# Kernel tuning notes

Hardware: AMD Instinct MI355X
Metric: run time of the kernel (lower is better)

## Reference

```python
import jax, jax.numpy as jnp
import numpy as np

NUM_HEADS = 16
NEG_INF = -1e30  # finite large negative; avoids NaN on fully-masked padded query rows


def setup_inputs() -> dict:
    key = jax.random.key(0)
    k0, k1, k2, k3 = jax.random.split(key, 4)
    B, S, E = 4, 2048, 1024
    x_padded = jax.random.normal(k0, (B, S, E), dtype=jnp.float32)
    # variable lengths in [S//2, S] so no batch row is fully empty
    seq_lengths = jax.random.randint(k1, (B,), S // 2, S + 1).astype(jnp.int32)
    Wqkv = jax.random.normal(k2, (3 * E, E), dtype=jnp.float32) * 0.02  # torch Linear weight [out,in]
    Wout = jax.random.normal(k3, (E, E), dtype=jnp.float32) * 0.02
    return {"x_padded": x_padded, "Wqkv": Wqkv, "Wout": Wout,
            "seq_lengths": seq_lengths, "window_left": 512, "window_right": 0}


def _build_mask(seq_lengths, S, window_left, window_right):
    # key-side padding mask: [B, S]
    pad = jnp.arange(S)[None, :] < seq_lengths[:, None]
    mask = pad[:, None, None, :]  # [B,1,1,S]
    if window_left >= 0 or window_right >= 0:
        i = jnp.arange(S)[:, None]
        j = jnp.arange(S)[None, :]
        win = jnp.ones((S, S), dtype=bool)
        if window_left >= 0:
            win = win & (j >= i - window_left)
        if window_right >= 0:
            win = win & (j <= i + window_right)
        mask = mask & win[None, None, :, :]
    elif (window_left, window_right) == (-1, 0):
        causal = jnp.tril(jnp.ones((S, S), dtype=bool))
        mask = mask & causal[None, None, :, :]
    return mask  # [B,1,S,S] (broadcasts over heads)


def reference(x_padded, Wqkv, Wout, seq_lengths, window_left, window_right):
    B, S, E = x_padded.shape
    H = NUM_HEADS
    D = E // H
    scale = 1.0 / jnp.sqrt(jnp.float32(D))
    qkv = x_padded @ Wqkv.T  # [B,S,3E]
    q, k, v = jnp.split(qkv, 3, axis=-1)
    q = q.reshape(B, S, H, D).transpose(0, 2, 1, 3)  # [B,H,S,D]
    k = k.reshape(B, S, H, D).transpose(0, 2, 1, 3)
    v = v.reshape(B, S, H, D).transpose(0, 2, 1, 3)
    mask = _build_mask(seq_lengths, S, window_left, window_right)
    scores = jnp.einsum("bhid,bhjd->bhij", q, k) * scale
    scores = jnp.where(mask, scores, NEG_INF)
    attn = jax.nn.softmax(scores, axis=-1)
    out = jnp.einsum("bhij,bhjd->bhid", attn, v)  # [B,H,S,D]
    out = out.transpose(0, 2, 1, 3).reshape(B, S, E)
    return out @ Wout.T
```

## Files before the change

### kernel.cpp

```cpp
#include <hip/hip_runtime.h>

typedef __bf16 bf16;
typedef __attribute__((ext_vector_type(2))) __bf16 bf16x2;
typedef __attribute__((ext_vector_type(4))) __bf16 bf16x4;
typedef __attribute__((ext_vector_type(8))) __bf16 bf16x8;
typedef __attribute__((ext_vector_type(4))) float f32x4;
typedef __attribute__((ext_vector_type(16))) float f32x16;

#define B_ 4
#define S_ 2048
#define H_ 16
#define D_ 64
#define E_ 1024

#define BM 256
#define BN 128
#define BK 64

__device__ __forceinline__ int imin(int a, int b) { return a < b ? a : b; }
__device__ __forceinline__ int imax(int a, int b) { return a > b ? a : b; }

__device__ __forceinline__ void gload_lds16(const void* g, void* l) {
  __builtin_amdgcn_global_load_lds(
      (const __attribute__((address_space(1))) void*)g,
      (__attribute__((address_space(3))) void*)l, 16, 0, 0);
}

__global__ __launch_bounds__(256) void cvt3_kernel(
    const float* __restrict__ x, bf16* __restrict__ xb,
    const float* __restrict__ wqkv, bf16* __restrict__ wqkvb,
    const float* __restrict__ wout, bf16* __restrict__ woutb) {
  const int bid = blockIdx.x;
  const float* in;
  bf16* out;
  int idx;
  if (bid < 4096) { in = x; out = xb; idx = bid; }
  else if (bid < 5632) { in = wqkv; out = wqkvb; idx = bid - 4096; }
  else { in = wout; out = woutb; idx = bid - 5632; }
  const int i = (idx * 256 + threadIdx.x) * 8;
  float4 v0 = *(const float4*)(in + i);
  float4 v1 = *(const float4*)(in + i + 4);
  bf16x8 o;
  o[0] = (bf16)v0.x; o[1] = (bf16)v0.y; o[2] = (bf16)v0.z; o[3] = (bf16)v0.w;
  o[4] = (bf16)v1.x; o[5] = (bf16)v1.y; o[6] = (bf16)v1.z; o[7] = (bf16)v1.w;
  *(bf16x8*)(out + i) = o;
}

__global__ __launch_bounds__(512, 1) void gemm_pipe(
    const bf16* __restrict__ A, const bf16* __restrict__ Bm,
    int M, int N, int K, int mode,
    bf16* __restrict__ qd, bf16* __restrict__ kd, bf16* __restrict__ vtd,
    float* __restrict__ outf) {
  __shared__ __align__(16) bf16 As[3][BM * BK];
  __shared__ __align__(16) bf16 Bs[3][BN * BK];
  const int tid = threadIdx.x;
  const int wave = tid >> 6, lane = tid & 63;
  const int l15 = lane & 15, l4 = lane >> 4;
  const int wm = (wave >> 1) * 64;
  const int wn = (wave & 1) * 64;

  const int nwg = gridDim.x * gridDim.y;
  const int fid = blockIdx.y * gridDim.x + blockIdx.x;
  const int chunk = nwg >> 3;
  const int swz = (fid & 7) * chunk + (fid >> 3);
  const int tn = swz % gridDim.x;
  const int tm = swz / gridDim.x;

  const bf16* Abase = A + (size_t)tm * BM * K;
  const bf16* Bbase = Bm + (size_t)tn * BN * K;

  f32x4 acc[4][4];
#pragma unroll
  for (int i = 0; i < 4; ++i)
#pragma unroll
    for (int j = 0; j < 4; ++j)
#pragma unroll
      for (int r = 0; r < 4; ++r) acc[i][j][r] = 0.f;

  const int NT = K >> 6;

#define STAGE_A(sbuf, k0)                                                      \
  {                                                                            \
    _Pragma("unroll") for (int ld = 0; ld < 4; ++ld) {                         \
      const int idx = ld * 512 + tid;                                          \
      const int row = idx >> 3, g = idx & 7;                                   \
      const int gs = g ^ (row & 7);                                            \
      gload_lds16(Abase + (size_t)row * K + (k0) + gs * 8,                     \
                  As[sbuf] + (ld * 512 + wave * 64) * 8);                      \
    }                                                                          \
  }
#define STAGE_B(sbuf, k0)                                                      \
  {                                                                            \
    _Pragma("unroll") for (int ld = 0; ld < 2; ++ld) {                         \
      const int idx = ld * 512 + tid;                                          \
      const int row = idx >> 3, g = idx & 7;                                   \
      const int gs = g ^ (row & 7);                                            \
      gload_lds16(Bbase + (size_t)row * K + (k0) + gs * 8,                     \
                  Bs[sbuf] + (ld * 512 + wave * 64) * 8);                      \
    }                                                                          \
  }

  STAGE_A(0, 0); STAGE_B(0, 0);
  STAGE_A(1, BK); STAGE_B(1, BK);
  asm volatile("s_waitcnt vmcnt(6)" ::: "memory");
  __builtin_amdgcn_s_barrier();

  int p = 0;
  for (int t = 0; t < NT; ++t) {
    const bf16* Ap = As[p];
    const bf16* Bp = Bs[p];
    const int sb = (p + 2 >= 3) ? p - 1 : p + 2;
    const int sk0 = ((t + 2 < NT) ? t + 2 : NT - 1) * BK;

    bf16x8 a[4], bfr[4];
#pragma unroll
    for (int i = 0; i < 4; ++i) {
      const int ra = wm + i * 16 + l15;
      a[i] = *(const bf16x8*)(Ap + ra * 64 + ((l4 ^ (ra & 7)) * 8));
      const int rb = wn + i * 16 + l15;
      bfr[i] = *(const bf16x8*)(Bp + rb * 64 + ((l4 ^ (rb & 7)) * 8));
    }
    STAGE_A(sb, sk0);
    __builtin_amdgcn_s_setprio(1);
#pragma unroll
    for (int i = 0; i < 4; ++i)
#pragma unroll
      for (int j = 0; j < 4; ++j)
        acc[i][j] = __builtin_amdgcn_mfma_f32_16x16x32_bf16(a[i], bfr[j],
                                                            acc[i][j], 0, 0, 0);
    __builtin_amdgcn_s_setprio(0);
#pragma unroll
    for (int i = 0; i < 4; ++i) {
      const int ra = wm + i * 16 + l15;
      a[i] = *(const bf16x8*)(Ap + ra * 64 + (((4 + l4) ^ (ra & 7)) * 8));
      const int rb = wn + i * 16 + l15;
      bfr[i] = *(const bf16x8*)(Bp + rb * 64 + (((4 + l4) ^ (rb & 7)) * 8));
    }
    STAGE_B(sb, sk0);
    __builtin_amdgcn_s_setprio(1);
#pragma unroll
    for (int i = 0; i < 4; ++i)
#pragma unroll
      for (int j = 0; j < 4; ++j)
        acc[i][j] = __builtin_amdgcn_mfma_f32_16x16x32_bf16(a[i], bfr[j],
                                                            acc[i][j], 0, 0, 0);
    __builtin_amdgcn_s_setprio(0);

    asm volatile("s_waitcnt vmcnt(6)" ::: "memory");
    __builtin_amdgcn_s_barrier();
    p = (p + 1 >= 3) ? 0 : p + 1;
  }
#undef STAGE_A
#undef STAGE_B

  if (mode == 0) {
#pragma unroll
    for (int i = 0; i < 4; ++i) {
      const int m0 = tm * BM + wm + i * 16 + l4 * 4;
      const int b = m0 >> 11, s = m0 & (S_ - 1);
#pragma unroll
      for (int j = 0; j < 4; ++j) {
        const int n = tn * BN + wn + j * 16 + l15;
        const int which = n >> 10;
        const int hn = n & 1023;
        const int h = hn >> 6, d = hn & 63;
        const f32x4 av = acc[i][j];
        if (which == 0) {
#pragma unroll
          for (int r = 0; r < 4; ++r)
            qd[((size_t)(b * H_ + h) * S_ + (s + r)) * D_ + d] =
                (bf16)(av[r] * 0.125f);
        } else if (which == 1) {
#pragma unroll
          for (int r = 0; r < 4; ++r)
            kd[((size_t)(b * H_ + h) * S_ + (s + r)) * D_ + d] = (bf16)av[r];
        } else {
          bf16x4 pv;
#pragma unroll
          for (int r = 0; r < 4; ++r) pv[r] = (bf16)av[r];
          *(bf16x4*)(vtd + ((size_t)(b * H_ + h) * D_ + d) * S_ + s) = pv;
        }
      }
    }
  } else {
#pragma unroll
    for (int i = 0; i < 4; ++i) {
      const int m0 = tm * BM + wm + i * 16 + l4 * 4;
#pragma unroll
      for (int j = 0; j < 4; ++j) {
        const int n = tn * BN + wn + j * 16 + l15;
#pragma unroll
        for (int r = 0; r < 4; ++r) outf[(size_t)(m0 + r) * N + n] = acc[i][j][r];
      }
    }
  }
}

__global__ __launch_bounds__(256) void meanv_kernel(const bf16* __restrict__ vt,
                                                    float* __restrict__ meanv) {
  const int bh = blockIdx.x >> 2, dq = blockIdx.x & 3;
  const int tid = threadIdx.x;
  const int dl = tid >> 4;
  const int sl = tid & 15;
  const int d = dq * 16 + dl;
  const bf16* row = vt + ((size_t)bh * D_ + d) * S_;
  float s = 0.f;
#pragma unroll
  for (int it = 0; it < 16; ++it) {
    bf16x8 v = *(const bf16x8*)(row + it * 128 + sl * 8);
#pragma unroll
    for (int j = 0; j < 8; ++j) s += (float)v[j];
  }
#pragma unroll
  for (int m = 1; m < 16; m <<= 1) s += __shfl_xor(s, m, 64);
  if (sl == 0) meanv[(size_t)bh * D_ + d] = s * (1.0f / (float)S_);
}

__device__ __forceinline__ int pk2(float a, float b) {
  union { bf16x2 h; int i; } u;
  u.h[0] = (bf16)a; u.h[1] = (bf16)b;
  return u.i;
}

__global__ __launch_bounds__(256) void attn_kernel(
    const bf16* __restrict__ q, const bf16* __restrict__ k,
    const bf16* __restrict__ vt, const float* __restrict__ meanv,
    const int* __restrict__ seq_lengths, const int* __restrict__ wlp,
    const int* __restrict__ wrp, bf16* __restrict__ attn_out) {
  __shared__ __align__(16) bf16 Ks[2][128 * 64];
  __shared__ __align__(16) bf16 Vs[2][64 * 128];
  const int tid = threadIdx.x, wave = tid >> 6, lane = tid & 63;
  const int l31 = lane & 31, l5 = lane >> 5;
  const int bid0 = blockIdx.x;
  const int bid = (bid0 & 7) * 64 + (bid0 >> 3);
  const int bh = bid >> 3;
  const int gp = bid & 7;
  const int b = bh >> 4, h = bh & 15;
  const int seq_len = seq_lengths[b];
  const int wl = wlp[0], wr = wrp[0];

  const bf16* qbase = q + (size_t)bh * S_ * D_;
  const bf16* kbase = k + (size_t)bh * S_ * D_;
  const bf16* vtb = vt + (size_t)bh * D_ * S_;

#define STAGE(bufb, kt0)                                                       \
  {                                                                            \
    _Pragma("unroll") for (int ld = 0; ld < 4; ++ld) {                         \
      const int idx = ld * 256 + tid;                                          \
      const int krow_i = idx >> 3, kg_ = idx & 7;                              \
      const int kgs = kg_ ^ (krow_i & 7);                                      \
      const int krow = imin((kt0) + krow_i, S_ - 1);                           \
      gload_lds16(kbase + (size_t)krow * 64 + kgs * 8, Ks[bufb] + idx * 8);    \
      const int vrow = idx >> 4, vg_ = idx & 15;                               \
      const int vgs = vg_ ^ (vrow & 15);                                       \
      const int vcol = imin((kt0) + vgs * 8, S_ - 8);                          \
      gload_lds16(vtb + (size_t)vrow * S_ + vcol, Vs[bufb] + idx * 8);         \
    }                                                                          \
  }
#define LDS_K(bufb, row, gran)                                                 \
  (*(const bf16x8*)((const char*)(Ks[bufb]) + (row) * 128 +                    \
                    (((gran) ^ ((row) & 7)) << 4)))
#define LDS_V(bufb, row, gran)                                                 \
  (*(const bf16x8*)((const char*)(Vs[bufb]) + (row) * 256 +                    \
                    (((gran) ^ ((row) & 15)) << 4)))

  for (int seg = 0; seg < 2; ++seg) {
    const int g = seg ? (15 - gp) : gp;
    const int q0b = g * 128;
    const int q0w = q0b + wave * 32;

    bf16x8 qa[4];
#pragma unroll
    for (int dg = 0; dg < 4; ++dg)
      qa[dg] = *(const bf16x8*)(qbase + (size_t)(q0w + l31) * D_ +
                                dg * 16 + l5 * 8);

    const int hi_blk = (wr >= 0) ? imin(q0b + 127 + wr, S_ - 1) : (S_ - 1);
    const int end_blk = imin(hi_blk + 1, seq_len);
    const int lo_blk = (wl >= 0) ? imax(0, q0b - wl) : 0;
    const int beg_blk = lo_blk & ~127;
    const int ntb = (end_blk > beg_blk) ? ((end_blk - beg_blk + 127) >> 7) : 0;

    const int w_hi = (wr >= 0) ? (q0w + 31 + wr) : (S_ - 1);
    const int w_end = imin(w_hi + 1, seq_len);
    const int w_lo = (wl >= 0) ? imax(0, q0w - wl) : 0;

    f32x16 o0, o1;
#pragma unroll
    for (int r = 0; r < 16; ++r) { o0[r] = 0.f; o1[r] = 0.f; }
    float mrun = -1e30f, lrun = 0.f;

    if (ntb > 0) STAGE(0, beg_blk);
    __syncthreads();

    for (int t = 0; t < ntb; ++t) {
      const int kt = beg_blk + t * 128;
      if (t + 1 < ntb) STAGE((t + 1) & 1, kt + 128);
      const int bufb = t & 1;

#pragma unroll
      for (int kk = 0; kk < 2; ++kk) {
        const int kts = kt + kk * 64;
        const bool active = (kts < w_end) && (kts + 63 >= w_lo);
        if (active) {
          f32x16 sf0, sf1;
#pragma unroll
          for (int r = 0; r < 16; ++r) { sf0[r] = 0.f; sf1[r] = 0.f; }
#pragma unroll
          for (int dg = 0; dg < 4; ++dg) {
            bf16x8 kb0 = LDS_K(bufb, kk * 64 + l31, dg * 2 + l5);
            bf16x8 kb1 = LDS_K(bufb, kk * 64 + 32 + l31, dg * 2 + l5);
            sf0 = __builtin_amdgcn_mfma_f32_32x32x16_bf16(kb0, qa[dg], sf0,
                                                          0, 0, 0);
            sf1 = __builtin_amdgcn_mfma_f32_32x32x16_bf16(kb1, qa[dg], sf1,
                                                          0, 0, 0);
          }

          bool allv = (kts + 63 < seq_len);
          if (wr >= 0) allv = allv && (kts + 63 <= q0w + wr);
          if (wl >= 0) allv = allv && (kts >= q0w + 31 - wl);
          if (!allv) {
            const int qrow = q0w + l31;
#pragma unroll
            for (int hh = 0; hh < 2; ++hh)
#pragma unroll
              for (int r = 0; r < 16; ++r) {
                const int key = kts + hh * 32 + (r & 3) + 8 * (r >> 2) + 4 * l5;
                bool valid = (key < seq_len);
                if (wr >= 0) valid = valid && (key <= qrow + wr);
                if (wl >= 0) valid = valid && (key >= qrow - wl);
                if (hh == 0) sf0[r] = valid ? sf0[r] : -1e30f;
                else sf1[r] = valid ? sf1[r] : -1e30f;
              }
          }
          float tmax = -1e30f;
#pragma unroll
          for (int r = 0; r < 16; ++r) {
            tmax = fmaxf(tmax, sf0[r]);
            tmax = fmaxf(tmax, sf1[r]);
          }
          tmax = fmaxf(tmax, __shfl_xor(tmax, 32, 64));

          if (!__all(tmax <= mrun + 8.0f)) {
            const float mnew = fmaxf(mrun, tmax);
            const float corr = __expf(mrun - mnew);
            mrun = mnew;
            lrun *= corr;
#pragma unroll
            for (int r = 0; r < 16; ++r) { o0[r] *= corr; o1[r] *= corr; }
          }

          float lsum = 0.f;
#pragma unroll
          for (int r = 0; r < 16; ++r) {
            const float e0 = (sf0[r] <= -1e29f) ? 0.f : __expf(sf0[r] - mrun);
            const float e1 = (sf1[r] <= -1e29f) ? 0.f : __expf(sf1[r] - mrun);
            sf0[r] = e0; sf1[r] = e1;
            lsum += e0 + e1;
          }
          lsum += __shfl_xor(lsum, 32, 64);
          lrun += lsum;

          bf16x8 pb[4];
#pragma unroll
          for (int kg = 0; kg < 4; ++kg) {
            const int base = (kg & 1) * 8;
            float p0, p1, p2, p3, p4, p5, p6, p7;
            if (kg < 2) {
              p0 = sf0[base + 0]; p1 = sf0[base + 1]; p2 = sf0[base + 2];
              p3 = sf0[base + 3]; p4 = sf0[base + 4]; p5 = sf0[base + 5];
              p6 = sf0[base + 6]; p7 = sf0[base + 7];
            } else {
              p0 = sf1[base + 0]; p1 = sf1[base + 1]; p2 = sf1[base + 2];
              p3 = sf1[base + 3]; p4 = sf1[base + 4]; p5 = sf1[base + 5];
              p6 = sf1[base + 6]; p7 = sf1[base + 7];
            }
            const int w0 = pk2(p0, p1);
            const int w1 = pk2(p2, p3);
            const int w2 = pk2(p4, p5);
            const int w3 = pk2(p6, p7);
            auto r02 = __builtin_amdgcn_permlane32_swap(w0, w2, false, false);
            auto r13 = __builtin_amdgcn_permlane32_swap(w1, w3, false, false);
            union { int i[4]; bf16x8 v; } u;
            u.i[0] = r02[0]; u.i[1] = r13[0]; u.i[2] = r02[1]; u.i[3] = r13[1];
            pb[kg] = u.v;
          }

#pragma unroll
          for (int kg = 0; kg < 4; ++kg) {
            bf16x8 va0 = LDS_V(bufb, l31, kk * 8 + kg * 2 + l5);
            bf16x8 va1 = LDS_V(bufb, 32 + l31, kk * 8 + kg * 2 + l5);
            o0 = __builtin_amdgcn_mfma_f32_32x32x16_bf16(va0, pb[kg], o0,
                                                         0, 0, 0);
            o1 = __builtin_amdgcn_mfma_f32_32x32x16_bf16(va1, pb[kg], o1,
                                                         0, 0, 0);
          }
        }
      }
      __syncthreads();
    }

    const int qrow = q0w + l31;
    bf16* outp = attn_out + ((size_t)(b * S_ + qrow)) * E_ + h * 64;
    if (lrun > 0.f) {
      const float inv = 1.0f / lrun;
#pragma unroll
      for (int dg2 = 0; dg2 < 2; ++dg2) {
        const f32x16& o = dg2 ? o1 : o0;
#pragma unroll
        for (int rg = 0; rg < 4; ++rg) {
          const int d0 = dg2 * 32 + 8 * rg + 4 * l5;
          bf16x4 ov;
#pragma unroll
          for (int j = 0; j < 4; ++j) ov[j] = (bf16)(o[rg * 4 + j] * inv);
          *(bf16x4*)(outp + d0) = ov;
        }
      }
    } else {
      const float* mv = meanv + (size_t)bh * D_;
#pragma unroll
      for (int dg2 = 0; dg2 < 2; ++dg2)
#pragma unroll
        for (int rg = 0; rg < 4; ++rg) {
          const int d0 = dg2 * 32 + 8 * rg + 4 * l5;
          bf16x4 ov;
#pragma unroll
          for (int j = 0; j < 4; ++j) ov[j] = (bf16)mv[d0 + j];
          *(bf16x4*)(outp + d0) = ov;
        }
    }
    __syncthreads();
  }
#undef STAGE
#undef LDS_K
#undef LDS_V
}

extern "C" void kernel_launch(void* const* d_in, const int* in_sizes, int n_in,
                              void* d_out, int out_size, void* d_ws, size_t ws_size,
                              hipStream_t stream) {
  const float* x = (const float*)d_in[0];
  const float* Wqkv = (const float*)d_in[1];
  const float* Wout = (const float*)d_in[2];
  const int* seq_lengths = (const int*)d_in[3];
  const int* wl = (const int*)d_in[4];
  const int* wr = (const int*)d_in[5];
  float* out = (float*)d_out;

  char* ws = (char*)d_ws;
  bf16* xb = (bf16*)ws;      ws += (size_t)8192 * 1024 * 2;
  bf16* wqkvb = (bf16*)ws;   ws += (size_t)3072 * 1024 * 2;
  bf16* woutb = (bf16*)ws;   ws += (size_t)1024 * 1024 * 2;
  bf16* qd = (bf16*)ws;      ws += (size_t)B_ * H_ * S_ * D_ * 2;
  bf16* kd = (bf16*)ws;      ws += (size_t)B_ * H_ * S_ * D_ * 2;
  bf16* vtd = (bf16*)ws;     ws += (size_t)B_ * H_ * S_ * D_ * 2;
  bf16* attn = (bf16*)ws;    ws += (size_t)8192 * 1024 * 2;
  float* meanv = (float*)ws; ws += (size_t)B_ * H_ * D_ * 4;

  cvt3_kernel<<<6144, 256, 0, stream>>>(x, xb, Wqkv, wqkvb, Wout, woutb);

  gemm_pipe<<<dim3(24, 32), 512, 0, stream>>>(xb, wqkvb, 8192, 3072, 1024, 0,
                                              qd, kd, vtd, nullptr);
  meanv_kernel<<<256, 256, 0, stream>>>(vtd, meanv);
  attn_kernel<<<512, 256, 0, stream>>>(qd, kd, vtd, meanv, seq_lengths, wl, wr,
                                       attn);
  gemm_pipe<<<dim3(8, 32), 512, 0, stream>>>(attn, woutb, 8192, 1024, 1024, 1,
                                             nullptr, nullptr, nullptr, out);
}
```

Before: 159.5 us.

## Fuse fp32-to-bf16 conversion of x into the QKV GEMM A-tile load

Stops converting the activation x to bf16 in a separate pass. The new QKV GEMM loads fp32 A tiles into registers, converts them and writes swizzled bf16 to LDS, while B still uses direct global-to-LDS loads. It also uses a custom tile-to-block mapping. This saves a 32MB fp32 read plus a 16MB bf16 write/read round trip, at the cost of double the A bytes per tile inside the GEMM, extra register pressure and VALU conversion work in the main loop.

Measured after the change: 179.6 us. +12.6%, slower.

```diff
diff --git a/kernel.cpp b/kernel.cpp
--- a/kernel.cpp
+++ b/kernel.cpp
@@ -26,17 +26,15 @@
       (__attribute__((address_space(3))) void*)l, 16, 0, 0);
 }
 
-__global__ __launch_bounds__(256) void cvt3_kernel(
-    const float* __restrict__ x, bf16* __restrict__ xb,
+__global__ __launch_bounds__(256) void cvt2_kernel(
     const float* __restrict__ wqkv, bf16* __restrict__ wqkvb,
     const float* __restrict__ wout, bf16* __restrict__ woutb) {
   const int bid = blockIdx.x;
   const float* in;
   bf16* out;
   int idx;
-  if (bid < 4096) { in = x; out = xb; idx = bid; }
-  else if (bid < 5632) { in = wqkv; out = wqkvb; idx = bid - 4096; }
-  else { in = wout; out = woutb; idx = bid - 5632; }
+  if (bid < 1536) { in = wqkv; out = wqkvb; idx = bid; }
+  else { in = wout; out = woutb; idx = bid - 1536; }
   const int i = (idx * 256 + threadIdx.x) * 8;
   float4 v0 = *(const float4*)(in + i);
   float4 v1 = *(const float4*)(in + i + 4);
@@ -44,6 +42,166 @@
   o[0] = (bf16)v0.x; o[1] = (bf16)v0.y; o[2] = (bf16)v0.z; o[3] = (bf16)v0.w;
   o[4] = (bf16)v1.x; o[5] = (bf16)v1.y; o[6] = (bf16)v1.z; o[7] = (bf16)v1.w;
   *(bf16x8*)(out + i) = o;
+}
+
+__global__ __launch_bounds__(512, 1) void gemm_qkv(
+    const float* __restrict__ A, const bf16* __restrict__ Bm,
+    int K,
+    bf16* __restrict__ qd, bf16* __restrict__ kd, bf16* __restrict__ vtd) {
+  __shared__ __align__(16) bf16 As[3][BM * BK];
+  __shared__ __align__(16) bf16 Bs[3][BN * BK];
+  const int tid = threadIdx.x;
+  const int wave = tid >> 6, lane = tid & 63;
+  const int l15 = lane & 15, l4 = lane >> 4;
+  const int wm = (wave >> 1) * 64;
+  const int wn = (wave & 1) * 64;
+
+  const int fid = blockIdx.y * gridDim.x + blockIdx.x;
+  const int x = fid & 7;
+  const int j = fid >> 3;
+  const int tm = (x & 3) * 8 + (j / 12);
+  const int tn = (x >> 2) * 12 + (j % 12);
+
+  const float* Abase = A + (size_t)tm * BM * K;
+  const bf16* Bbase = Bm + (size_t)tn * BN * K;
+
+  f32x4 acc[4][4];
+#pragma unroll
+  for (int i = 0; i < 4; ++i)
+#pragma unroll
+    for (int jj = 0; jj < 4; ++jj)
+#pragma unroll
+      for (int r = 0; r < 4; ++r) acc[i][jj][r] = 0.f;
+
+  const int NT = K >> 6;
+
+  float4 areg[4][2];
+
+#define LOADA(k0)                                                              \
+  {                                                                            \
+    _Pragma("unroll") for (int ld = 0; ld < 4; ++ld) {                         \
+      const int idx = ld * 512 + tid;                                          \
+      const int row = idx >> 3, g = idx & 7;                                   \
+      const int gs = g ^ (row & 7);                                            \
+      const float* src = Abase + (size_t)row * K + (k0) + gs * 8;              \
+      areg[ld][0] = *(const float4*)(src);                                     \
+      areg[ld][1] = *(const float4*)(src + 4);                                 \
+    }                                                                          \
+  }
+#define WRITEA(sbuf)                                                           \
+  {                                                                            \
+    _Pragma("unroll") for (int ld = 0; ld < 4; ++ld) {                         \
+      const int idx = ld * 512 + tid;                                          \
+      bf16x8 o;                                                                \
+      o[0] = (bf16)areg[ld][0].x; o[1] = (bf16)areg[ld][0].y;                  \
+      o[2] = (bf16)areg[ld][0].z; o[3] = (bf16)areg[ld][0].w;                  \
+      o[4] = (bf16)areg[ld][1].x; o[5] = (bf16)areg[ld][1].y;                  \
+      o[6] = (bf16)areg[ld][1].z; o[7] = (bf16)areg[ld][1].w;                  \
+      *(bf16x8*)(As[sbuf] + (size_t)idx * 8) = o;                              \
+    }                                                                          \
+  }
+#define STAGE_B(sbuf, k0)                                                      \
+  {                                                                            \
+    _Pragma("unroll") for (int ld = 0; ld < 2; ++ld) {                         \
+      const int idx = ld * 512 + tid;                                          \
+      const int row = idx >> 3, g = idx & 7;                                   \
+      const int gs = g ^ (row & 7);                                            \
+      gload_lds16(Bbase + (size_t)row * K + (k0) + gs * 8,                     \
+                  Bs[sbuf] + (ld * 512 + wave * 64) * 8);                      \
+    }                                                                          \
+  }
+
+  LOADA(0);
+  asm volatile("s_waitcnt vmcnt(0)" ::: "memory");
+  WRITEA(0);
+  LOADA(BK);
+  STAGE_B(0, 0);
+  STAGE_B(1, BK);
+  asm volatile("s_waitcnt vmcnt(4)" ::: "memory");
+  WRITEA(1);
+  asm volatile("s_waitcnt vmcnt(2) lgkmcnt(0)" ::: "memory");
+  __builtin_amdgcn_s_barrier();
+
+  int p = 0;
+  for (int t = 0; t < NT; ++t) {
+    const bf16* Ap = As[p];
+    const bf16* Bp = Bs[p];
+    const int sb = (p + 2 >= 3) ? p - 1 : p + 2;
+    const int sk0 = ((t + 2 < NT) ? t + 2 : NT - 1) * BK;
+
+    LOADA(sk0);
+
+    bf16x8 a[4], bfr[4];
+#pragma unroll
+    for (int i = 0; i < 4; ++i) {
+      const int ra = wm + i * 16 + l15;
+      a[i] = *(const bf16x8*)(Ap + ra * 64 + ((l4 ^ (ra & 7)) * 8));
+      const int rb = wn + i * 16 + l15;
+      bfr[i] = *(const bf16x8*)(Bp + rb * 64 + ((l4 ^ (rb & 7)) * 8));
+    }
+    __builtin_amdgcn_s_setprio(1);
+#pragma unroll
+    for (int i = 0; i < 4; ++i)
+#pragma unroll
+      for (int jj = 0; jj < 4; ++jj)
+        acc[i][jj] = __builtin_amdgcn_mfma_f32_16x16x32_bf16(a[i], bfr[jj],
+                                                             acc[i][jj], 0, 0, 0);
+    __builtin_amdgcn_s_setprio(0);
+#pragma unroll
+    for (int i = 0; i < 4; ++i) {
+      const int ra = wm + i * 16 + l15;
+      a[i] = *(const bf16x8*)(Ap + ra * 64 + (((4 + l4) ^ (ra & 7)) * 8));
+      const int rb = wn + i * 16 + l15;
+      bfr[i] = *(const bf16x8*)(Bp + rb * 64 + (((4 + l4) ^ (rb & 7)) * 8));
+    }
+    STAGE_B(sb, sk0);
+    __builtin_amdgcn_s_setprio(1);
+#pragma unroll
+    for (int i = 0; i < 4; ++i)
+#pragma unroll
+      for (int jj = 0; jj < 4; ++jj)
+        acc[i][jj] = __builtin_amdgcn_mfma_f32_16x16x32_bf16(a[i], bfr[jj],
+                                                             acc[i][jj], 0, 0, 0);
+    __builtin_amdgcn_s_setprio(0);
+
+    asm volatile("s_waitcnt vmcnt(2)" ::: "memory");
+    WRITEA(sb);
+    asm volatile("s_waitcnt lgkmcnt(0)" ::: "memory");
+    __builtin_amdgcn_s_barrier();
+    p = (p + 1 >= 3) ? 0 : p + 1;
+  }
+#undef LOADA
+#undef WRITEA
+#undef STAGE_B
+
+#pragma unroll
+  for (int i = 0; i < 4; ++i) {
+    const int m0 = tm * BM + wm + i * 16 + l4 * 4;
+    const int b = m0 >> 11, s = m0 & (S_ - 1);
+#pragma unroll
+    for (int jj = 0; jj < 4; ++jj) {
+      const int n = tn * BN + wn + jj * 16 + l15;
+      const int which = n >> 10;
+      const int hn = n & 1023;
+      const int h = hn >> 6, d = hn & 63;
+      const f32x4 av = acc[i][jj];
+      if (which == 0) {
+#pragma unroll
+        for (int r = 0; r < 4; ++r)
+          qd[((size_t)(b * H_ + h) * S_ + (s + r)) * D_ + d] =
+              (bf16)(av[r] * 0.125f);
+      } else if (which == 1) {
+#pragma unroll
+        for (int r = 0; r < 4; ++r)
+          kd[((size_t)(b * H_ + h) * S_ + (s + r)) * D_ + d] = (bf16)av[r];
+      } else {
+        bf16x4 pv;
+#pragma unroll
+        for (int r = 0; r < 4; ++r) pv[r] = (bf16)av[r];
+        *(bf16x4*)(vtd + ((size_t)(b * H_ + h) * D_ + d) * S_ + s) = pv;
+      }
+    }
+  }
 }
 
 __global__ __launch_bounds__(512, 1) void gemm_pipe(
@@ -59,8 +217,8 @@
   const int wm = (wave >> 1) * 64;
   const int wn = (wave & 1) * 64;
 
+  const int fid = blockIdx.y * gridDim.x + blockIdx.x;
   const int nwg = gridDim.x * gridDim.y;
-  const int fid = blockIdx.y * gridDim.x + blockIdx.x;
   const int chunk = nwg >> 3;
   const int swz = (fid & 7) * chunk + (fid >> 3);
   const int tn = swz % gridDim.x;
@@ -448,7 +606,6 @@
   float* out = (float*)d_out;
 
   char* ws = (char*)d_ws;
-  bf16* xb = (bf16*)ws;      ws += (size_t)8192 * 1024 * 2;
   bf16* wqkvb = (bf16*)ws;   ws += (size_t)3072 * 1024 * 2;
   bf16* woutb = (bf16*)ws;   ws += (size_t)1024 * 1024 * 2;
   bf16* qd = (bf16*)ws;      ws += (size_t)B_ * H_ * S_ * D_ * 2;
@@ -457,10 +614,9 @@
   bf16* attn = (bf16*)ws;    ws += (size_t)8192 * 1024 * 2;
   float* meanv = (float*)ws; ws += (size_t)B_ * H_ * D_ * 4;
 
-  cvt3_kernel<<<6144, 256, 0, stream>>>(x, xb, Wqkv, wqkvb, Wout, woutb);
-
-  gemm_pipe<<<dim3(24, 32), 512, 0, stream>>>(xb, wqkvb, 8192, 3072, 1024, 0,
-                                              qd, kd, vtd, nullptr);
+  cvt2_kernel<<<2048, 256, 0, stream>>>(Wqkv, wqkvb, Wout, woutb);
+
+  gemm_qkv<<<dim3(24, 32), 512, 0, stream>>>(x, wqkvb, 1024, qd, kd, vtd);
   meanv_kernel<<<256, 256, 0, stream>>>(vtd, meanv);
   attn_kernel<<<512, 256, 0, stream>>>(qd, kd, vtd, meanv, seq_lengths, wl, wr,
                                        attn);
```
